# Performance work log

Measured on AMD Instinct MI355X. Metric: run time of the kernel, lower is better.

The kernel has to match this reference:

```python
import jax, jax.numpy as jnp
import numpy as np


def _resize_axis_linear(x, new_size, axis):
    """1-D linear resize along `axis` with align_corners=True semantics."""
    old = x.shape[axis]
    if old == new_size:
        return x
    pos = jnp.arange(new_size, dtype=jnp.float32) * (float(old - 1) / float(max(new_size - 1, 1)))
    i0 = jnp.floor(pos).astype(jnp.int32)
    i1 = jnp.minimum(i0 + 1, old - 1)
    w = (pos - i0.astype(jnp.float32)).astype(x.dtype)
    shp = [1] * x.ndim
    shp[axis] = new_size
    w = w.reshape(shp)
    return jnp.take(x, i0, axis=axis) * (1 - w) + jnp.take(x, i1, axis=axis) * w


def bilinear_resize(x, out_h, out_w):
    # x: (B, h, w, C) -> (B, out_h, out_w, C), align_corners=True
    x = _resize_axis_linear(x, out_h, axis=1)
    x = _resize_axis_linear(x, out_w, axis=2)
    return x


def grid_sample_bilinear_border(feat, grid):
    """feat: (B,H,W,C); grid: (B,H',W',2) with (x,y) in [-1,1]; align_corners=True, border padding."""
    B, H, W, C = feat.shape
    ix = (grid[..., 0] + 1.0) * 0.5 * (W - 1)
    iy = (grid[..., 1] + 1.0) * 0.5 * (H - 1)
    ix = jnp.clip(ix, 0.0, W - 1)  # border padding
    iy = jnp.clip(iy, 0.0, H - 1)
    ix0 = jnp.floor(ix).astype(jnp.int32)
    iy0 = jnp.floor(iy).astype(jnp.int32)
    ix1 = jnp.minimum(ix0 + 1, W - 1)
    iy1 = jnp.minimum(iy0 + 1, H - 1)
    wx = (ix - ix0.astype(ix.dtype))[..., None]
    wy = (iy - iy0.astype(iy.dtype))[..., None]
    b = jnp.arange(B)[:, None, None]
    v00 = feat[b, iy0, ix0]
    v01 = feat[b, iy0, ix1]
    v10 = feat[b, iy1, ix0]
    v11 = feat[b, iy1, ix1]
    top = v00 * (1 - wx) + v01 * wx
    bot = v10 * (1 - wx) + v11 * wx
    return top * (1 - wy) + bot * wy


def _forward(features, H, W, W1, b1, W2, b2, weight_coef, pool_size=2):
    B, L, C = features.shape
    # ---- pool_patches: avg_pool2d(kernel=stride=pool_size) on (B,H,W,C) ----
    feat_map = features.reshape(B, H, W, C)
    Hp, Wp = H // pool_size, W // pool_size
    pooled = feat_map.reshape(B, Hp, pool_size, Wp, pool_size, C).mean(axis=(2, 4))  # (B,Hp,Wp,C)
    Lp = Hp * Wp
    pooled_flat = pooled.reshape(B, Lp, C)
    # ---- deform predictor MLP (GELU exact, matches torch default) ----
    h = jax.nn.gelu(pooled_flat @ W1 + b1, approximate=False)
    dp = (h @ W2 + b2) * weight_coef  # (B, Lp, 4)
    delta_x = jnp.tanh(dp[..., 0])
    delta_y = jnp.tanh(dp[..., 1])
    delta_w = jax.nn.softplus(dp[..., 2])
    delta_h = jax.nn.softplus(dp[..., 3])
    # ---- base normalized grid at pooled resolution ----
    gy, gx = jnp.meshgrid(jnp.arange(Hp, dtype=jnp.float32), jnp.arange(Wp, dtype=jnp.float32), indexing='ij')
    gx = 2.0 * gx / max(Wp - 1, 1) - 1.0
    gy = 2.0 * gy / max(Hp - 1, 1) - 1.0
    ox = gx.reshape(1, Lp)
    oy = gy.reshape(1, Lp)
    dx = jnp.clip(ox + delta_x * (2.0 / max(Wp, 1)), -1.0, 1.0)
    dy = jnp.clip(oy + delta_y * (2.0 / max(Hp, 1)), -1.0, 1.0)
    deformed_coords = jnp.stack([dx, dy], axis=-1)  # (B, Lp, 2)
    # ---- upsample coords to full res and grid-sample features ----
    coords_map = deformed_coords.reshape(B, Hp, Wp, 2)
    coords_full = bilinear_resize(coords_map, H, W)  # (B, H, W, 2)
    sampled = grid_sample_bilinear_border(feat_map, coords_full)  # (B, H, W, C)
    deformed_features = sampled.reshape(B, L, C)
    full_deform_params = jnp.stack([delta_x, delta_y, delta_w, delta_h], axis=-1)  # (B, Lp, 4)
    return deformed_features, full_deform_params, deformed_coords


def setup_inputs() -> dict:
    key = jax.random.key(0)
    ks = jax.random.split(key, 6)
    B, H, W, C = 16, 128, 128, 192
    hidden = max(C // 4, 64)
    features = jax.random.normal(ks[0], (B, H * W, C), dtype=jnp.float32)
    W1 = jax.random.normal(ks[1], (C, hidden), dtype=jnp.float32) * (1.0 / np.sqrt(C))
    b1 = jax.random.normal(ks[2], (hidden,), dtype=jnp.float32) * 0.01
    W2 = jax.random.normal(ks[3], (hidden, 4), dtype=jnp.float32) * (1.0 / np.sqrt(hidden))
    b2 = jax.random.normal(ks[4], (4,), dtype=jnp.float32) * 0.01
    weight_coef = jnp.ones((4,), dtype=jnp.float32)
    return {"features": features, "H": H, "W": W, "W1": W1, "b1": b1, "W2": W2, "b2": b2, "weight_coef": weight_coef}


def reference(features, H, W, W1, b1, W2, b2, weight_coef):
    return _forward(features, H, W, W1, b1, W2, b2, weight_coef)
```

## Files before the change

kernel.cpp:

```cpp
#include <hip/hip_runtime.h>
#include <math.h>

#define Bn   16
#define Hn   128
#define Wn   128
#define Cn   192
#define HPn  64
#define WPn  64
#define LPn  4096
#define Ln   16384
#define HIDn 64

__device__ __forceinline__ float gelu_exact(float x) {
    return 0.5f * x * (1.0f + erff(x * 0.70710678118654752440f));
}
__device__ __forceinline__ float softplus_f(float x) {
    return fmaxf(x, 0.0f) + log1pf(expf(-fabsf(x)));
}

__global__ __launch_bounds__(256)
void pool_mlp_kernel(const float* __restrict__ feat,
                     const float* __restrict__ W1,
                     const float* __restrict__ b1,
                     const float* __restrict__ W2,
                     const float* __restrict__ b2,
                     const float* __restrict__ wcoef,
                     float* __restrict__ out_params,
                     float* __restrict__ out_coords)
{
    __shared__ float s_pool[16][Cn];
    __shared__ float s_hid[16][HIDn];
    const int t = threadIdx.x;
    const int g0  = blockIdx.x * 16;
    const int b   = g0 >> 12;
    const int lp0 = g0 & 4095;
    const int hp  = lp0 >> 6;
    const int wp0 = lp0 & 63;

    const float* fb = feat + (size_t)b * Ln * Cn;
    const int h0 = hp * 2;

#pragma unroll
    for (int k = 0; k < 12; ++k) {
        int v = t + k * 256;
        int p = v / Cn;
        int c = v - p * Cn;
        int w0 = (wp0 + p) * 2;
        size_t base = ((size_t)h0 * Wn + w0) * Cn + c;
        float s = fb[base] + fb[base + Cn] + fb[base + (size_t)Wn * Cn] +
                  fb[base + (size_t)Wn * Cn + Cn];
        s_pool[p][c] = 0.25f * s;
    }
    __syncthreads();

    const int j  = t & 63;
    const int pb = t >> 6;
    float a0 = b1[j], a1 = a0, a2 = a0, a3 = a0;
    for (int c = 0; c < Cn; ++c) {
        float w = W1[c * HIDn + j];
        a0 = fmaf(s_pool[pb     ][c], w, a0);
        a1 = fmaf(s_pool[pb +  4][c], w, a1);
        a2 = fmaf(s_pool[pb +  8][c], w, a2);
        a3 = fmaf(s_pool[pb + 12][c], w, a3);
    }
    s_hid[pb     ][j] = gelu_exact(a0);
    s_hid[pb +  4][j] = gelu_exact(a1);
    s_hid[pb +  8][j] = gelu_exact(a2);
    s_hid[pb + 12][j] = gelu_exact(a3);
    __syncthreads();

    if (t < 64) {
        int p = t >> 2, k = t & 3;
        float acc = b2[k];
        for (int c = 0; c < HIDn; ++c)
            acc = fmaf(s_hid[p][c], W2[c * 4 + k], acc);
        float dp = acc * wcoef[k];
        float val = (k < 2) ? tanhf(dp) : softplus_f(dp);
        int lp = lp0 + p;
        out_params[((size_t)b * LPn + lp) * 4 + k] = val;
        if (k == 0) {
            float ox = 2.0f * (float)(wp0 + p) / 63.0f - 1.0f;
            float dx = ox + val * (2.0f / 64.0f);
            dx = fminf(fmaxf(dx, -1.0f), 1.0f);
            out_coords[((size_t)b * LPn + lp) * 2 + 0] = dx;
        } else if (k == 1) {
            float oy = 2.0f * (float)hp / 63.0f - 1.0f;
            float dy = oy + val * (2.0f / 64.0f);
            dy = fminf(fmaxf(dy, -1.0f), 1.0f);
            out_coords[((size_t)b * LPn + lp) * 2 + 1] = dy;
        }
    }
}

__global__ __launch_bounds__(256)
void sample_kernel(const float* __restrict__ feat,
                   const float* __restrict__ coords,
                   float* __restrict__ out)
{
    const int idx = blockIdx.x * 256 + threadIdx.x;
    const int pix = idx / 48;
    const int c4  = idx - pix * 48;
    const int b   = pix >> 14;
    const int rem = pix & 16383;
    const int i   = rem >> 7;
    const int jj  = rem & 127;

    const float sc = 63.0f / 127.0f;
    float py = i * sc, px = jj * sc;
    float fy0 = floorf(py), fx0 = floorf(px);
    float wy = py - fy0, wx = px - fx0;
    int iy0 = (int)fy0, ix0 = (int)fx0;
    int iy1 = min(iy0 + 1, 63), ix1 = min(ix0 + 1, 63);
    const float2* cm = (const float2*)coords + ((size_t)b << 12);
    float2 c00 = cm[iy0 * 64 + ix0];
    float2 c01 = cm[iy0 * 64 + ix1];
    float2 c10 = cm[iy1 * 64 + ix0];
    float2 c11 = cm[iy1 * 64 + ix1];
    float gx = (c00.x * (1.0f - wy) + c10.x * wy) * (1.0f - wx) +
               (c01.x * (1.0f - wy) + c11.x * wy) * wx;
    float gy = (c00.y * (1.0f - wy) + c10.y * wy) * (1.0f - wx) +
               (c01.y * (1.0f - wy) + c11.y * wy) * wx;

    float ix = (gx + 1.0f) * 0.5f * 127.0f;
    float iy = (gy + 1.0f) * 0.5f * 127.0f;
    ix = fminf(fmaxf(ix, 0.0f), 127.0f);
    iy = fminf(fmaxf(iy, 0.0f), 127.0f);
    float fx = floorf(ix), fy = floorf(iy);
    float swx = ix - fx, swy = iy - fy;
    int sx0 = (int)fx, sy0 = (int)fy;
    int sx1 = min(sx0 + 1, 127), sy1 = min(sy0 + 1, 127);

    const float4* f4 = (const float4*)feat + ((size_t)b << 14) * 48;
    float4 v00 = f4[(sy0 * 128 + sx0) * 48 + c4];
    float4 v01 = f4[(sy0 * 128 + sx1) * 48 + c4];
    float4 v10 = f4[(sy1 * 128 + sx0) * 48 + c4];
    float4 v11 = f4[(sy1 * 128 + sx1) * 48 + c4];

    float iwx = 1.0f - swx, iwy = 1.0f - swy;
    float4 r;
    r.x = (v00.x * iwx + v01.x * swx) * iwy + (v10.x * iwx + v11.x * swx) * swy;
    r.y = (v00.y * iwx + v01.y * swx) * iwy + (v10.y * iwx + v11.y * swx) * swy;
    r.z = (v00.z * iwx + v01.z * swx) * iwy + (v10.z * iwx + v11.z * swx) * swy;
    r.w = (v00.w * iwx + v01.w * swx) * iwy + (v10.w * iwx + v11.w * swx) * swy;
    ((float4*)out)[idx] = r;
}

extern "C" void kernel_launch(void* const* d_in, const int* in_sizes, int n_in,
                              void* d_out, int out_size, void* d_ws, size_t ws_size,
                              hipStream_t stream) {
    const float* feat = (const float*)d_in[0];
    const float* W1 = (const float*)d_in[3];
    const float* b1 = (const float*)d_in[4];
    const float* W2 = (const float*)d_in[5];
    const float* b2 = (const float*)d_in[6];
    const float* wc = (const float*)d_in[7];

    float* out        = (float*)d_out;
    float* out_params = out + (size_t)Bn * Ln * Cn;
    float* out_coords = out_params + (size_t)Bn * LPn * 4;

    pool_mlp_kernel<<<(Bn * LPn) / 16, 256, 0, stream>>>(
        feat, W1, b1, W2, b2, wc, out_params, out_coords);

    sample_kernel<<<(Bn * Hn * Wn * 48) / 256, 256, 0, stream>>>(
        feat, out_coords, out);
}
```

Measured before the change: 411.1 us.

## Vectorize pooling loads and compute sampling coordinates once per row in shared memory

The pooling stage now reads features as float4 and stores pooled values as float4 in shared memory, so the MLP inner loop walks four channels per step. The sample kernel now uses one block per output row. Per-pixel offsets and weights are computed once by 128 threads and shared, where before every one of the 48 channel-threads of a pixel recomputed them. The shared-memory setup adds a barrier and leaves half the threads idle during it, and each block now launches with 24 float4 outputs per thread.

```diff
diff --git a/kernel.cpp b/kernel.cpp
--- a/kernel.cpp
+++ b/kernel.cpp
@@ -5,6 +5,7 @@
 #define Hn   128
 #define Wn   128
 #define Cn   192
+#define C4n  48
 #define HPn  64
 #define WPn  64
 #define LPn  4096
@@ -28,8 +29,8 @@
                      float* __restrict__ out_params,
                      float* __restrict__ out_coords)
 {
-    __shared__ float s_pool[16][Cn];
-    __shared__ float s_hid[16][HIDn];
+    __shared__ float4 s_pool[16][C4n];
+    __shared__ float  s_hid[16][HIDn + 1];
     const int t = threadIdx.x;
     const int g0  = blockIdx.x * 16;
     const int b   = g0 >> 12;
@@ -37,31 +38,43 @@
     const int hp  = lp0 >> 6;
     const int wp0 = lp0 & 63;
 
-    const float* fb = feat + (size_t)b * Ln * Cn;
+    const float4* fb4 = (const float4*)feat + (size_t)b * Ln * C4n;
     const int h0 = hp * 2;
 
 #pragma unroll
-    for (int k = 0; k < 12; ++k) {
-        int v = t + k * 256;
-        int p = v / Cn;
-        int c = v - p * Cn;
+    for (int k = 0; k < 3; ++k) {
+        int v  = t + k * 256;
+        int p  = v / C4n;
+        int c4 = v - p * C4n;
         int w0 = (wp0 + p) * 2;
-        size_t base = ((size_t)h0 * Wn + w0) * Cn + c;
-        float s = fb[base] + fb[base + Cn] + fb[base + (size_t)Wn * Cn] +
-                  fb[base + (size_t)Wn * Cn + Cn];
-        s_pool[p][c] = 0.25f * s;
+        size_t base = ((size_t)h0 * Wn + w0) * C4n + c4;
+        float4 x00 = fb4[base];
+        float4 x01 = fb4[base + C4n];
+        float4 x10 = fb4[base + (size_t)Wn * C4n];
+        float4 x11 = fb4[base + (size_t)Wn * C4n + C4n];
+        float4 r;
+        r.x = 0.25f * (x00.x + x01.x + x10.x + x11.x);
+        r.y = 0.25f * (x00.y + x01.y + x10.y + x11.y);
+        r.z = 0.25f * (x00.z + x01.z + x10.z + x11.z);
+        r.w = 0.25f * (x00.w + x01.w + x10.w + x11.w);
+        s_pool[p][c4] = r;
     }
     __syncthreads();
 
     const int j  = t & 63;
     const int pb = t >> 6;
     float a0 = b1[j], a1 = a0, a2 = a0, a3 = a0;
-    for (int c = 0; c < Cn; ++c) {
-        float w = W1[c * HIDn + j];
-        a0 = fmaf(s_pool[pb     ][c], w, a0);
-        a1 = fmaf(s_pool[pb +  4][c], w, a1);
-        a2 = fmaf(s_pool[pb +  8][c], w, a2);
-        a3 = fmaf(s_pool[pb + 12][c], w, a3);
+    for (int c4 = 0; c4 < C4n; ++c4) {
+        float4 p0 = s_pool[pb     ][c4];
+        float4 p1 = s_pool[pb +  4][c4];
+        float4 p2 = s_pool[pb +  8][c4];
+        float4 p3 = s_pool[pb + 12][c4];
+        const float* wr = W1 + (c4 * 4) * HIDn + j;
+        float w0 = wr[0], w1 = wr[HIDn], w2 = wr[2 * HIDn], w3 = wr[3 * HIDn];
+        a0 = fmaf(p0.w, w3, fmaf(p0.z, w2, fmaf(p0.y, w1, fmaf(p0.x, w0, a0))));
+        a1 = fmaf(p1.w, w3, fmaf(p1.z, w2, fmaf(p1.y, w1, fmaf(p1.x, w0, a1))));
+        a2 = fmaf(p2.w, w3, fmaf(p2.z, w2, fmaf(p2.y, w1, fmaf(p2.x, w0, a2))));
+        a3 = fmaf(p3.w, w3, fmaf(p3.z, w2, fmaf(p3.y, w1, fmaf(p3.x, w0, a3))));
     }
     s_hid[pb     ][j] = gelu_exact(a0);
     s_hid[pb +  4][j] = gelu_exact(a1);
@@ -97,52 +110,67 @@
                    const float* __restrict__ coords,
                    float* __restrict__ out)
 {
-    const int idx = blockIdx.x * 256 + threadIdx.x;
-    const int pix = idx / 48;
-    const int c4  = idx - pix * 48;
-    const int b   = pix >> 14;
-    const int rem = pix & 16383;
-    const int i   = rem >> 7;
-    const int jj  = rem & 127;
+    __shared__ int   s_off[4][Wn];
+    __shared__ float s_wx[Wn];
+    __shared__ float s_wy[Wn];
+    const int t = threadIdx.x;
+    const int b = blockIdx.x >> 7;
+    const int i = blockIdx.x & 127;
 
-    const float sc = 63.0f / 127.0f;
-    float py = i * sc, px = jj * sc;
-    float fy0 = floorf(py), fx0 = floorf(px);
-    float wy = py - fy0, wx = px - fx0;
-    int iy0 = (int)fy0, ix0 = (int)fx0;
-    int iy1 = min(iy0 + 1, 63), ix1 = min(ix0 + 1, 63);
-    const float2* cm = (const float2*)coords + ((size_t)b << 12);
-    float2 c00 = cm[iy0 * 64 + ix0];
-    float2 c01 = cm[iy0 * 64 + ix1];
-    float2 c10 = cm[iy1 * 64 + ix0];
-    float2 c11 = cm[iy1 * 64 + ix1];
-    float gx = (c00.x * (1.0f - wy) + c10.x * wy) * (1.0f - wx) +
-               (c01.x * (1.0f - wy) + c11.x * wy) * wx;
-    float gy = (c00.y * (1.0f - wy) + c10.y * wy) * (1.0f - wx) +
-               (c01.y * (1.0f - wy) + c11.y * wy) * wx;
+    if (t < Wn) {
+        const int jj = t;
+        const float sc = 63.0f / 127.0f;
+        float py = i * sc, px = jj * sc;
+        float fy0 = floorf(py), fx0 = floorf(px);
+        float wy = py - fy0, wx = px - fx0;
+        int iy0 = (int)fy0, ix0 = (int)fx0;
+        int iy1 = min(iy0 + 1, 63), ix1 = min(ix0 + 1, 63);
+        const float2* cm = (const float2*)coords + ((size_t)b << 12);
+        float2 c00 = cm[iy0 * 64 + ix0];
+        float2 c01 = cm[iy0 * 64 + ix1];
+        float2 c10 = cm[iy1 * 64 + ix0];
+        float2 c11 = cm[iy1 * 64 + ix1];
+        float gx = (c00.x * (1.0f - wy) + c10.x * wy) * (1.0f - wx) +
+                   (c01.x * (1.0f - wy) + c11.x * wy) * wx;
+        float gy = (c00.y * (1.0f - wy) + c10.y * wy) * (1.0f - wx) +
+                   (c01.y * (1.0f - wy) + c11.y * wy) * wx;
+        float ixf = (gx + 1.0f) * 0.5f * 127.0f;
+        float iyf = (gy + 1.0f) * 0.5f * 127.0f;
+        ixf = fminf(fmaxf(ixf, 0.0f), 127.0f);
+        iyf = fminf(fmaxf(iyf, 0.0f), 127.0f);
+        float fx = floorf(ixf), fy = floorf(iyf);
+        int sx0 = (int)fx, sy0 = (int)fy;
+        int sx1 = min(sx0 + 1, 127), sy1 = min(sy0 + 1, 127);
+        s_off[0][jj] = (sy0 * Wn + sx0) * C4n;
+        s_off[1][jj] = (sy0 * Wn + sx1) * C4n;
+        s_off[2][jj] = (sy1 * Wn + sx0) * C4n;
+        s_off[3][jj] = (sy1 * Wn + sx1) * C4n;
+        s_wx[jj] = ixf - fx;
+        s_wy[jj] = iyf - fy;
+    }
+    __syncthreads();
 
-    float ix = (gx + 1.0f) * 0.5f * 127.0f;
-    float iy = (gy + 1.0f) * 0.5f * 127.0f;
-    ix = fminf(fmaxf(ix, 0.0f), 127.0f);
-    iy = fminf(fmaxf(iy, 0.0f), 127.0f);
-    float fx = floorf(ix), fy = floorf(iy);
-    float swx = ix - fx, swy = iy - fy;
-    int sx0 = (int)fx, sy0 = (int)fy;
-    int sx1 = min(sx0 + 1, 127), sy1 = min(sy0 + 1, 127);
+    const float4* f4 = (const float4*)feat + ((size_t)b << 14) * C4n;
+    float4* o4 = (float4*)out + (((size_t)b << 14) + (size_t)i * Wn) * C4n;
 
-    const float4* f4 = (const float4*)feat + ((size_t)b << 14) * 48;
-    float4 v00 = f4[(sy0 * 128 + sx0) * 48 + c4];
-    float4 v01 = f4[(sy0 * 128 + sx1) * 48 + c4];
-    float4 v10 = f4[(sy1 * 128 + sx0) * 48 + c4];
-    float4 v11 = f4[(sy1 * 128 + sx1) * 48 + c4];
-
-    float iwx = 1.0f - swx, iwy = 1.0f - swy;
-    float4 r;
-    r.x = (v00.x * iwx + v01.x * swx) * iwy + (v10.x * iwx + v11.x * swx) * swy;
-    r.y = (v00.y * iwx + v01.y * swx) * iwy + (v10.y * iwx + v11.y * swx) * swy;
-    r.z = (v00.z * iwx + v01.z * swx) * iwy + (v10.z * iwx + v11.z * swx) * swy;
-    r.w = (v00.w * iwx + v01.w * swx) * iwy + (v10.w * iwx + v11.w * swx) * swy;
-    ((float4*)out)[idx] = r;
+#pragma unroll 4
+    for (int k = 0; k < 24; ++k) {
+        int v  = t + k * 256;
+        int p  = v / C4n;
+        int c4 = v - p * C4n;
+        float swx = s_wx[p], swy = s_wy[p];
+        float4 v00 = f4[s_off[0][p] + c4];
+        float4 v01 = f4[s_off[1][p] + c4];
+        float4 v10 = f4[s_off[2][p] + c4];
+        float4 v11 = f4[s_off[3][p] + c4];
+        float iwx = 1.0f - swx, iwy = 1.0f - swy;
+        float4 r;
+        r.x = (v00.x * iwx + v01.x * swx) * iwy + (v10.x * iwx + v11.x * swx) * swy;
+        r.y = (v00.y * iwx + v01.y * swx) * iwy + (v10.y * iwx + v11.y * swx) * swy;
+        r.z = (v00.z * iwx + v01.z * swx) * iwy + (v10.z * iwx + v11.z * swx) * swy;
+        r.w = (v00.w * iwx + v01.w * swx) * iwy + (v10.w * iwx + v11.w * swx) * swy;
+        o4[v] = r;
+    }
 }
 
 extern "C" void kernel_launch(void* const* d_in, const int* in_sizes, int n_in,
@@ -162,6 +190,5 @@
     pool_mlp_kernel<<<(Bn * LPn) / 16, 256, 0, stream>>>(
         feat, W1, b1, W2, b2, wc, out_params, out_coords);
 
-    sample_kernel<<<(Bn * Hn * Wn * 48) / 256, 256, 0, stream>>>(
-        feat, out_coords, out);
+    sample_kernel<<<Bn * Hn, 256, 0, stream>>>(feat, out_coords, out);
 }
```

Result: slower. 432.4 us (+5.2%).
